# Kernel optimization log

Measured on AMD Instinct MI355X. Metric: run time of the kernel, lower is better.

Reference implementation:

```python
import jax, jax.numpy as jnp
import numpy as np

B, S, D, H = 64, 128, 1024, 512
N = 2 * S - 1          # total tree nodes (leaves + internal)
NSTEP = S - 1          # number of binary compositions
NW, NP = 511, 152      # word / phrase category counts


def _l2n(x):
    return x / jnp.clip(jnp.linalg.norm(x, axis=-1, keepdims=True), 1e-12)


def circular_correlation(a, b):
    a, b = _l2n(a), _l2n(b)
    c = jnp.fft.irfft(jnp.conj(jnp.fft.rfft(a)) * jnp.fft.rfft(b), n=H)
    return _l2n(c)


def _lstm_dir(x, w_ih, w_hh, b):
    # x: [B,S,D] -> hs: [B,S,H]; PyTorch gate order i,f,g,o
    xp = jnp.einsum('bsd,gd->bsg', x, w_ih) + b  # precompute input proj

    def step(carry, xt):
        h, c = carry
        g = xt + h @ w_hh.T
        i, f, gg, o = jnp.split(g, 4, axis=-1)
        c = jax.nn.sigmoid(f) * c + jax.nn.sigmoid(i) * jnp.tanh(gg)
        h = jax.nn.sigmoid(o) * jnp.tanh(c)
        return (h, c), h

    h0 = jnp.zeros((x.shape[0], H), x.dtype)
    _, hs = jax.lax.scan(step, (h0, h0), xp.transpose(1, 0, 2))
    return hs.transpose(1, 0, 2)


def setup_inputs():
    key = jax.random.key(0)
    ks = jax.random.split(key, 12)
    sc = 0.05
    elmo_rep = jax.random.normal(ks[0], (B, S, D), jnp.float32)
    w_ih_f = jax.random.normal(ks[1], (4 * H, D), jnp.float32) * sc
    w_hh_f = jax.random.normal(ks[2], (4 * H, H), jnp.float32) * sc
    b_f = jnp.zeros((4 * H,), jnp.float32)
    w_ih_b = jax.random.normal(ks[3], (4 * H, D), jnp.float32) * sc
    w_hh_b = jax.random.normal(ks[4], (4 * H, H), jnp.float32) * sc
    b_b = jnp.zeros((4 * H,), jnp.float32)
    W1 = jax.random.normal(ks[5], (H, H), jnp.float32) * sc
    W2 = jax.random.normal(ks[6], (H, H), jnp.float32) * sc
    word_W = jax.random.normal(ks[7], (NW, H), jnp.float32) * sc
    word_b = jnp.zeros((NW,), jnp.float32)
    phrase_W = jax.random.normal(ks[8], (NP, H), jnp.float32) * sc
    phrase_b = jnp.zeros((NP,), jnp.float32)
    # valid binary-tree composition schedule: parent S+i, children < S+i
    rng = np.random.default_rng(0)
    comp = np.zeros((B, NSTEP, 4), np.int32)
    comp[:, :, 0] = 2
    for i in range(NSTEP):
        comp[:, i, 1] = S + i
        comp[:, i, 2] = rng.integers(0, S + i, size=B)
        comp[:, i, 3] = rng.integers(0, S + i, size=B)
    composition_info = jnp.asarray(comp)
    pos = jnp.stack([jnp.arange(S), jnp.arange(S)], axis=1).astype(jnp.int32)
    original_pos = jnp.tile(pos[None], (B, 1, 1))
    batch_label = jax.random.randint(ks[9], (B, N), 0, NW, dtype=jnp.int64)
    return dict(elmo_rep=elmo_rep, w_ih_f=w_ih_f, w_hh_f=w_hh_f, b_f=b_f,
                w_ih_b=w_ih_b, w_hh_b=w_hh_b, b_b=b_b, W1=W1, W2=W2,
                word_W=word_W, word_b=word_b, phrase_W=phrase_W,
                phrase_b=phrase_b, composition_info=composition_info,
                original_pos=original_pos, batch_label=batch_label)


def reference(elmo_rep, w_ih_f, w_hh_f, b_f, w_ih_b, w_hh_b, b_b, W1, W2,
              word_W, word_b, phrase_W, phrase_b, composition_info,
              original_pos, batch_label):
    # BiLSTM over ELMo reps (all sequences full length S)
    fwd = _lstm_dir(elmo_rep, w_ih_f, w_hh_f, b_f)
    bwd = _lstm_dir(elmo_rep[:, ::-1], w_ih_b, w_hh_b, b_b)[:, ::-1]
    combined = jax.nn.leaky_relu(fwd @ W1.T + bwd @ W2.T, negative_slope=0.01)

    # scatter leaves into node buffer [B,N,H], then L2-normalize
    bidx = jnp.arange(B)[:, None]
    tgt = original_pos[:, :, 0]
    src = original_pos[:, :, 1]
    vector = jnp.zeros((B, N, H), combined.dtype)
    vector = vector.at[bidx, tgt].set(combined[bidx, src])
    vector = _l2n(vector)

    # sequential per-depth compose: gather children, circular-correlate, scatter parent
    b = jnp.arange(B)

    def step(vec, info):  # info: [B,4] = [type, parent, left, right]
        t, p, l, r = info[:, 0], info[:, 1], info[:, 2], info[:, 3]
        lv = vec[b, l]
        rv = vec[b, r]
        comp = circular_correlation(lv, rv)
        cur = vec[b, p]
        val = jnp.where((t == 1)[:, None], lv,
                        jnp.where((t == 2)[:, None], comp, cur))
        return vec.at[b, p].set(val), None

    vector, _ = jax.lax.scan(step, vector, composition_info.transpose(1, 0, 2))

    # words = leaf nodes (first S slots), phrases = internal nodes
    word_vector = vector[:, :S].reshape(-1, H)
    phrase_vector = vector[:, S:].reshape(-1, H)
    word_label = batch_label[:, :S].reshape(-1)
    phrase_label = batch_label[:, S:].reshape(-1)
    word_output = word_vector @ word_W.T + word_b
    phrase_output = phrase_vector @ phrase_W.T + phrase_b
    return word_output, phrase_output, word_label, phrase_label
```

## Files before the change

kernel.cpp:

```cpp
#include <hip/hip_runtime.h>
#include <math.h>

#define NB 64
#define NS 128
#define ND 1024
#define NH 512
#define NG 2048
#define NTOT 255
#define NSTEPS 127
#define NWV 511
#define NPV 152

static const size_t XPB_SZ = (size_t)2 * NS * NG * NB;
static const size_t H_SZ   = (size_t)2 * NS * NH * NB;
static const size_t VEC_SZ = (size_t)NB * NTOT * NH;
static const size_t HB_SZ  = (size_t)2 * NS * NH * NB;
static const size_t EB_SZ  = (size_t)NB * NS * ND;
static const size_t WB_SZ  = (size_t)4096 * ND;

typedef __attribute__((ext_vector_type(8))) short short8v;
typedef __attribute__((ext_vector_type(8))) unsigned short ushort8v;
typedef __attribute__((ext_vector_type(4))) float float4v;

__device__ __forceinline__ float sigm(float x) { return 1.f / (1.f + __expf(-x)); }
__device__ __forceinline__ float tanh_fast(float x) {
  const float e = __expf(2.f * x);
  return 1.f - 2.f / (e + 1.f);
}
__device__ __forceinline__ unsigned short f2bf(float x) {
  unsigned b = __float_as_uint(x);
  return (unsigned short)((b + 0x7FFFu + ((b >> 16) & 1u)) >> 16);
}
__device__ __forceinline__ float bf2f(unsigned short u) {
  return __uint_as_float(((unsigned)u) << 16);
}

#define FMA4x4(acc, av, bv)                                                    \
  acc[0][0] += av.x * bv.x; acc[0][1] += av.x * bv.y;                          \
  acc[0][2] += av.x * bv.z; acc[0][3] += av.x * bv.w;                          \
  acc[1][0] += av.y * bv.x; acc[1][1] += av.y * bv.y;                          \
  acc[1][2] += av.y * bv.z; acc[1][3] += av.y * bv.w;                          \
  acc[2][0] += av.z * bv.x; acc[2][1] += av.z * bv.y;                          \
  acc[2][2] += av.z * bv.z; acc[2][3] += av.z * bv.w;                          \
  acc[3][0] += av.w * bv.x; acc[3][1] += av.w * bv.y;                          \
  acc[3][2] += av.w * bv.z; acc[3][3] += av.w * bv.w;

__global__ __launch_bounds__(256) void k_cvt(
    const float* __restrict__ elmo, const float* __restrict__ wf,
    const float* __restrict__ wb, unsigned short* __restrict__ elmo_bf,
    unsigned short* __restrict__ W_bf, int* __restrict__ bar) {
  const int gid = blockIdx.x * 256 + threadIdx.x;
  if (gid < 8192) bar[gid] = 0;
  const int NE4 = (NB * NS * ND) / 4;
  const int NW4 = (4096 * ND) / 4;
  const int NW4h = NW4 / 2;
  for (int i = gid; i < NE4 + NW4; i += gridDim.x * 256) {
    float4 v;
    unsigned short* dst;
    if (i < NE4) {
      const int e0 = i << 2;
      const int b = e0 >> 17;
      const int t = (e0 >> 10) & 127;
      const int k = e0 & 1023;
      v = *(const float4*)(elmo + e0);
      dst = elmo_bf + ((size_t)((t << 6) + b) << 10) + k;
    } else {
      const int j = i - NE4;
      v = (j < NW4h) ? *(const float4*)(wf + ((size_t)j << 2))
                     : *(const float4*)(wb + ((size_t)(j - NW4h) << 2));
      dst = W_bf + ((size_t)j << 2);
    }
    uint2 u;
    u.x = (unsigned)f2bf(v.x) | ((unsigned)f2bf(v.y) << 16);
    u.y = (unsigned)f2bf(v.z) | ((unsigned)f2bf(v.w) << 16);
    *(uint2*)dst = u;
  }
}

__global__ __launch_bounds__(256) void k_xp(
    const unsigned short* __restrict__ elmo_bf,
    const unsigned short* __restrict__ W_bf,
    const float* __restrict__ biasf, const float* __restrict__ biasb,
    unsigned short* __restrict__ xpb) {
  __shared__ unsigned short As[128 * 64];
  __shared__ unsigned short Bs[128 * 64];
  const int tid = threadIdx.x;
  const int n0 = blockIdx.x * 128;
  const int m0 = blockIdx.y * 128;
  const int wv = tid >> 6, lane = tid & 63;
  const int cl = lane & 15, bq = lane >> 4;
  const int wm = (wv >> 1) << 6;
  const int wn = (wv & 1) << 6;
  const int sr = tid >> 1, skc = (tid & 1) << 5;
  const unsigned short* asrc = elmo_bf + (size_t)(m0 + sr) * ND + skc;
  const unsigned short* bsrc = W_bf + (size_t)(n0 + sr) * ND + skc;
  const int sswz = (sr & 15) << 3;
  float4v acc[4][4];
#pragma unroll
  for (int nt = 0; nt < 4; ++nt) {
    const int n = n0 + wn + nt * 16 + cl;
    const float bv = (n < 2048) ? biasf[n] : biasb[n - 2048];
#pragma unroll
    for (int mt = 0; mt < 4; ++mt) acc[mt][nt] = (float4v){bv, bv, bv, bv};
  }
  for (int k0 = 0; k0 < ND; k0 += 64) {
    ushort8v av4[4], bv4[4];
#pragma unroll
    for (int i = 0; i < 4; ++i) av4[i] = *(const ushort8v*)(asrc + k0 + 8 * i);
#pragma unroll
    for (int i = 0; i < 4; ++i) bv4[i] = *(const ushort8v*)(bsrc + k0 + 8 * i);
    __syncthreads();
#pragma unroll
    for (int i = 0; i < 4; ++i) {
      *(ushort8v*)&As[((sr << 6) + skc + 8 * i) ^ sswz] = av4[i];
      *(ushort8v*)&Bs[((sr << 6) + skc + 8 * i) ^ sswz] = bv4[i];
    }
    __syncthreads();
#pragma unroll
    for (int ks = 0; ks < 2; ++ks) {
      const int koff = (ks << 5) + (bq << 3);
      short8v af[4], bf_[4];
#pragma unroll
      for (int mt = 0; mt < 4; ++mt) {
        const int ar = wm + mt * 16 + cl;
        af[mt] = *(const short8v*)&As[((ar << 6) + koff) ^ ((ar & 15) << 3)];
      }
#pragma unroll
      for (int nt = 0; nt < 4; ++nt) {
        const int br = wn + nt * 16 + cl;
        bf_[nt] = *(const short8v*)&Bs[((br << 6) + koff) ^ ((br & 15) << 3)];
      }
#pragma unroll
      for (int mt = 0; mt < 4; ++mt)
#pragma unroll
        for (int nt = 0; nt < 4; ++nt)
          acc[mt][nt] =
              __builtin_amdgcn_mfma_f32_16x16x32_bf16(af[mt], bf_[nt], acc[mt][nt], 0, 0, 0);
    }
  }
#pragma unroll
  for (int mt = 0; mt < 4; ++mt) {
    const int mbase = m0 + wm + mt * 16 + (bq << 2);
    const int t = mbase >> 6, b4 = mbase & 63;
#pragma unroll
    for (int nt = 0; nt < 4; ++nt) {
      const int n = n0 + wn + nt * 16 + cl;
      const int dir = n >> 11, grow = n & 2047;
      const int g = grow >> 9, cb = (grow & 511) >> 4;
      const float4v a = acc[mt][nt];
      uint2 u;
      u.x = (unsigned)f2bf(a[0]) | ((unsigned)f2bf(a[1]) << 16);
      u.y = (unsigned)f2bf(a[2]) | ((unsigned)f2bf(a[3]) << 16);
      const size_t idx =
          ((((size_t)(dir * NS + t) * 32 + cb) * 4 + g) << 10) + (cl << 6) + b4;
      *(uint2*)&xpb[idx] = u;
    }
  }
}

__global__ __launch_bounds__(256) void k_lstm(
    const float* __restrict__ whh_f, const float* __restrict__ whh_b,
    const unsigned short* __restrict__ xpb, float* __restrict__ h_all,
    unsigned short* __restrict__ h_bf, int* __restrict__ bar) {
  __shared__ unsigned short WS[64 * 512];
  __shared__ unsigned short hOut[64 * 16];
  const int bid = blockIdx.x;
  const int dir = bid >> 5;
  const int cb = bid & 31;
  const int col0 = cb << 4;
  const int tid = threadIdx.x;
  const int lane = tid & 63;
  const int w = tid >> 6;
  const int cl = lane & 15, bq = lane >> 4;
  const int b4 = (w << 4) + (bq << 2);
  const int arow = (w << 4) + cl;
  const float* whh = dir ? whh_b : whh_f;

  {
    const int gr = tid >> 2;
    const int kc = (tid & 3) << 7;
    const int gg = gr >> 4, cc = gr & 15;
    const float* src = whh + (size_t)(gg * NH + col0 + cc) * NH + kc;
    const int swz = (gr & 15) << 3;
#pragma unroll
    for (int i = 0; i < 16; ++i) {
      const float4 f0 = *(const float4*)(src + 8 * i);
      const float4 f1 = *(const float4*)(src + 8 * i + 4);
      ushort8v u;
      u[0] = f2bf(f0.x); u[1] = f2bf(f0.y); u[2] = f2bf(f0.z); u[3] = f2bf(f0.w);
      u[4] = f2bf(f1.x); u[5] = f2bf(f1.y); u[6] = f2bf(f1.z); u[7] = f2bf(f1.w);
      *(ushort8v*)&WS[((gr << 9) + kc + 8 * i) ^ swz] = u;
    }
  }
  __syncthreads();

  float* hd = h_all + (size_t)dir * NS * NH * NB;
  unsigned short* hb_us = h_bf + ((size_t)dir * NS << 15);
  unsigned long long* hb_ull = (unsigned long long*)h_bf + ((size_t)dir * NS << 12);

  float4v c4 = {0.f, 0.f, 0.f, 0.f};

  uint2 xg0, xg1, xg2, xg3;
  {
    const int pos0 = dir ? (NS - 1) : 0;
    const unsigned short* xc = xpb + (((size_t)(dir * NS + pos0) * 32 + cb) << 12);
    xg0 = *(const uint2*)&xc[(0 << 10) + (cl << 6) + b4];
    xg1 = *(const uint2*)&xc[(1 << 10) + (cl << 6) + b4];
    xg2 = *(const uint2*)&xc[(2 << 10) + (cl << 6) + b4];
    xg3 = *(const uint2*)&xc[(3 << 10) + (cl << 6) + b4];
  }

  for (int t = 0; t < NS; ++t) {
    const int pos = dir ? (NS - 1 - t) : t;
    float4v acc[4] = {{0.f, 0.f, 0.f, 0.f}, {0.f, 0.f, 0.f, 0.f},
                      {0.f, 0.f, 0.f, 0.f}, {0.f, 0.f, 0.f, 0.f}};
    if (t > 0) {
      const int prevpos = dir ? (pos + 1) : (pos - 1);
      const unsigned long long* hsrc = hb_ull + ((size_t)prevpos << 13);
      unsigned long long ha0[16], ha1[16];
#pragma unroll
      for (int ks = 0; ks < 16; ++ks) {
        const int uidx = (arow << 7) + (ks << 3) + (bq << 1);
        ha0[ks] = __hip_atomic_load(&hsrc[uidx], __ATOMIC_RELAXED,
                                    __HIP_MEMORY_SCOPE_AGENT);
        ha1[ks] = __hip_atomic_load(&hsrc[uidx + 1], __ATOMIC_RELAXED,
                                    __HIP_MEMORY_SCOPE_AGENT);
      }
#pragma unroll
      for (int ks = 0; ks < 16; ++ks) {
        union { unsigned long long u[2]; short8v v; } au;
        au.u[0] = ha0[ks]; au.u[1] = ha1[ks];
        const short8v a = au.v;
        const int koff = (ks << 5) + (bq << 3);
#pragma unroll
        for (int g = 0; g < 4; ++g) {
          const short8v bb =
              *(const short8v*)&WS[((((g << 4) + cl) << 9) + koff) ^ (cl << 3)];
          acc[g] = __builtin_amdgcn_mfma_f32_16x16x32_bf16(a, bb, acc[g], 0, 0, 0);
        }
      }
    }
    float hv[4];
#pragma unroll
    for (int i = 0; i < 4; ++i) {
      const unsigned xw0 = (i < 2) ? xg0.x : xg0.y;
      const unsigned xw1 = (i < 2) ? xg1.x : xg1.y;
      const unsigned xw2 = (i < 2) ? xg2.x : xg2.y;
      const unsigned xw3 = (i < 2) ? xg3.x : xg3.y;
      const int sh = (i & 1) << 4;
      const float gi = sigm(acc[0][i] + bf2f((unsigned short)(xw0 >> sh)));
      const float gf = sigm(acc[1][i] + bf2f((unsigned short)(xw1 >> sh)));
      const float gc = tanh_fast(acc[2][i] + bf2f((unsigned short)(xw2 >> sh)));
      const float go = sigm(acc[3][i] + bf2f((unsigned short)(xw3 >> sh)));
      c4[i] = gf * c4[i] + gi * gc;
      hv[i] = go * tanh_fast(c4[i]);
    }
    *(float4*)(hd + ((size_t)pos * NH + col0 + cl) * NB + b4) =
        make_float4(hv[0], hv[1], hv[2], hv[3]);
    if (t < NS - 1) {
#pragma unroll
      for (int i = 0; i < 4; ++i) hOut[((b4 + i) << 4) + cl] = f2bf(hv[i]);
      const int npos = dir ? (pos - 1) : (pos + 1);
      const unsigned short* xc =
          xpb + (((size_t)(dir * NS + npos) * 32 + cb) << 12);
      const uint2 nx0 = *(const uint2*)&xc[(0 << 10) + (cl << 6) + b4];
      const uint2 nx1 = *(const uint2*)&xc[(1 << 10) + (cl << 6) + b4];
      const uint2 nx2 = *(const uint2*)&xc[(2 << 10) + (cl << 6) + b4];
      const uint2 nx3 = *(const uint2*)&xc[(3 << 10) + (cl << 6) + b4];
      __syncthreads();
      if (tid < 128) {
        const int bb = tid >> 1, half = tid & 1;
        const unsigned long long v =
            *(const unsigned long long*)&hOut[(bb << 4) + (half << 3)];
        __hip_atomic_store(
            (unsigned long long*)&hb_us[((size_t)pos << 15) + (bb << 9) + col0 +
                                        (half << 3)],
            v, __ATOMIC_RELAXED, __HIP_MEMORY_SCOPE_AGENT);
      }
      __syncthreads();
      if (tid == 0) {
        int* ctr = &bar[(((t << 1) + dir) << 5)];
        __hip_atomic_fetch_add(ctr, 1, __ATOMIC_RELAXED, __HIP_MEMORY_SCOPE_AGENT);
        while (__hip_atomic_load(ctr, __ATOMIC_RELAXED, __HIP_MEMORY_SCOPE_AGENT) < 32) {
        }
      }
      __syncthreads();
      xg0 = nx0; xg1 = nx1; xg2 = nx2; xg3 = nx3;
    }
  }
}

__global__ __launch_bounds__(256) void k_comb(
    const float* __restrict__ h_all, const float* __restrict__ W1,
    const float* __restrict__ W2, float* __restrict__ vec) {
  __shared__ float A1[16][68], A2[16][68], B1[16][68], B2[16][68];
  const int tid = threadIdx.x;
  const int n0 = blockIdx.x * 64;
  const int s = blockIdx.y;
  const float* h0 = h_all + (size_t)s * NH * NB;
  const float* h1 = h_all + ((size_t)NS + s) * NH * NB;
  const int aj = tid >> 4, ai4 = (tid & 15) << 2;
  const int lr = tid >> 2, lc4 = (tid & 3) << 2;
  const int tx = tid & 15, ty = tid >> 4;
  const float* b1row = W1 + (size_t)(n0 + lr) * NH;
  const float* b2row = W2 + (size_t)(n0 + lr) * NH;
  float acc[4][4] = {};
  for (int k0 = 0; k0 < NH; k0 += 16) {
    *(float4*)&A1[aj][ai4] = *(const float4*)(h0 + (size_t)(k0 + aj) * NB + ai4);
    *(float4*)&A2[aj][ai4] = *(const float4*)(h1 + (size_t)(k0 + aj) * NB + ai4);
    const float4 w1 = *(const float4*)(b1row + k0 + lc4);
    B1[lc4 + 0][lr] = w1.x; B1[lc4 + 1][lr] = w1.y;
    B1[lc4 + 2][lr] = w1.z; B1[lc4 + 3][lr] = w1.w;
    const float4 w2 = *(const float4*)(b2row + k0 + lc4);
    B2[lc4 + 0][lr] = w2.x; B2[lc4 + 1][lr] = w2.y;
    B2[lc4 + 2][lr] = w2.z; B2[lc4 + 3][lr] = w2.w;
    __syncthreads();
#pragma unroll
    for (int kk = 0; kk < 16; ++kk) {
      const float4 a1 = *(const float4*)&A1[kk][ty << 2];
      const float4 b1 = *(const float4*)&B1[kk][tx << 2];
      FMA4x4(acc, a1, b1)
      const float4 a2 = *(const float4*)&A2[kk][ty << 2];
      const float4 b2 = *(const float4*)&B2[kk][tx << 2];
      FMA4x4(acc, a2, b2)
    }
    __syncthreads();
  }
#pragma unroll
  for (int i = 0; i < 4; ++i) {
    const int b = (ty << 2) + i;
#pragma unroll
    for (int j = 0; j < 4; ++j) {
      const int nn = n0 + (tx << 2) + j;
      float v = acc[i][j];
      v = v > 0.f ? v : 0.01f * v;
      vec[((size_t)b * NTOT + s) * NH + nn] = v;
    }
  }
}

__global__ __launch_bounds__(256) void k_norm(float* __restrict__ vec) {
  const int row = (blockIdx.x << 2) + (threadIdx.x >> 6);
  const int lane = threadIdx.x & 63;
  const int b = row >> 7, s = row & 127;
  float* p = vec + ((size_t)b * NTOT + s) * NH;
  float4 v0 = *(float4*)(p + (lane << 3));
  float4 v1 = *(float4*)(p + (lane << 3) + 4);
  float ss = v0.x * v0.x + v0.y * v0.y + v0.z * v0.z + v0.w * v0.w +
             v1.x * v1.x + v1.y * v1.y + v1.z * v1.z + v1.w * v1.w;
#pragma unroll
  for (int off = 32; off; off >>= 1) ss += __shfl_down(ss, off);
  ss = __shfl(ss, 0);
  const float sc = 1.f / fmaxf(sqrtf(ss), 1e-12f);
  v0.x *= sc; v0.y *= sc; v0.z *= sc; v0.w *= sc;
  v1.x *= sc; v1.y *= sc; v1.z *= sc; v1.w *= sc;
  *(float4*)(p + (lane << 3)) = v0;
  *(float4*)(p + (lane << 3) + 4) = v1;
}

#define SKW(f) ((f) + (((f) >> 5) << 2))
__global__ __launch_bounds__(512) void k_compose(
    float* __restrict__ vec, const int* __restrict__ cinfo) {
  __shared__ float lv[512];
  __shared__ float rvd[1152];
  __shared__ float cpart[8 * 576];
  __shared__ float red[8];
  const int b = blockIdx.x;
  const int tid = threadIdx.x;
  float* vb = vec + (size_t)b * NTOT * NH;
  const int* ib = cinfo + b * NSTEPS * 4;
  const int jq = tid >> 6;
  const int jb = jq << 6;
  const int k8 = (tid & 63) << 3;
  const int wid = tid >> 6, lane = tid & 63;
  for (int i = 0; i < NSTEPS; ++i) {
    const int tt = ib[i * 4 + 0], p = ib[i * 4 + 1];
    const int l = ib[i * 4 + 2], r = ib[i * 4 + 3];
    const float lvv = vb[(size_t)l * NH + tid];
    const float rvv = vb[(size_t)r * NH + tid];
    lv[tid] = lvv;
    rvd[SKW(tid)] = rvv;
    rvd[SKW(512 + tid)] = rvv;
    __syncthreads();
    if (tt == 2) {
      float acc[8] = {};
#pragma unroll 4
      for (int jj = 0; jj < 64; jj += 4) {
        const int j = jb + jj;
        const float4 l4 = *(const float4*)&lv[j];
        const int f0 = j + k8;
        const float4 r0 = *(const float4*)&rvd[SKW(f0)];
        const float4 r1 = *(const float4*)&rvd[SKW(f0 + 4)];
        const float4 r2 = *(const float4*)&rvd[SKW(f0 + 8)];
        const float rw[12] = {r0.x, r0.y, r0.z, r0.w, r1.x, r1.y,
                              r1.z, r1.w, r2.x, r2.y, r2.z, r2.w};
#pragma unroll
        for (int kk = 0; kk < 8; ++kk)
          acc[kk] += l4.x * rw[kk] + l4.y * rw[kk + 1] + l4.z * rw[kk + 2] +
                     l4.w * rw[kk + 3];
      }
      const int ca = jq * 576 + SKW(k8);
      *(float4*)&cpart[ca] = make_float4(acc[0], acc[1], acc[2], acc[3]);
      *(float4*)&cpart[ca + 4] = make_float4(acc[4], acc[5], acc[6], acc[7]);
    }
    __syncthreads();
    float ck = 0.f;
    if (tt == 2) {
      const int ra = SKW(tid);
#pragma unroll
      for (int q = 0; q < 8; ++q) ck += cpart[q * 576 + ra];
    }
    float ss = ck * ck;
#pragma unroll
    for (int off = 32; off; off >>= 1) ss += __shfl_xor(ss, off);
    if (lane == 0) red[wid] = ss;
    __syncthreads();
    if (tt == 2) {
      const float tot = red[0] + red[1] + red[2] + red[3] +
                        red[4] + red[5] + red[6] + red[7];
      const float inv = 1.f / fmaxf(sqrtf(tot), 1e-12f);
      vb[(size_t)p * NH + tid] = ck * inv;
    } else if (tt == 1) {
      vb[(size_t)p * NH + tid] = lvv;
    }
    __syncthreads();
  }
}

template <int MODE>
__global__ __launch_bounds__(256) void k_out(
    const float* __restrict__ vec, const float* __restrict__ W,
    const float* __restrict__ bias, float* __restrict__ out) {
  constexpr int NOUT = MODE ? NPV : NWV;
  __shared__ float As[16][68], Bs[16][68];
  const int tid = threadIdx.x;
  const int n0 = blockIdx.x * 64, m0 = blockIdx.y * 64;
  const int lr = tid >> 2, lc4 = (tid & 3) << 2;
  const int tx = tid & 15, ty = tid >> 4;
  const int m = m0 + lr;
  int vr;
  if (MODE == 0) {
    vr = (m >> 7) * NTOT + (m & 127);
  } else {
    const int bb = m / 127;
    vr = bb * NTOT + NS + (m - bb * 127);
  }
  const float* arow = vec + (size_t)vr * NH;
  const int n = n0 + lr;
  const float* brow = W + (size_t)n * NH;
  const bool bok = (n < NOUT);
  float acc[4][4] = {};
  for (int k0 = 0; k0 < NH; k0 += 16) {
    const float4 a4 = *(const float4*)(arow + k0 + lc4);
    As[lc4 + 0][lr] = a4.x; As[lc4 + 1][lr] = a4.y;
    As[lc4 + 2][lr] = a4.z; As[lc4 + 3][lr] = a4.w;
    float4 b4 = make_float4(0.f, 0.f, 0.f, 0.f);
    if (bok) b4 = *(const float4*)(brow + k0 + lc4);
    Bs[lc4 + 0][lr] = b4.x; Bs[lc4 + 1][lr] = b4.y;
    Bs[lc4 + 2][lr] = b4.z; Bs[lc4 + 3][lr] = b4.w;
    __syncthreads();
#pragma unroll
    for (int kk = 0; kk < 16; ++kk) {
      const float4 av = *(const float4*)&As[kk][ty << 2];
      const float4 bv = *(const float4*)&Bs[kk][tx << 2];
      FMA4x4(acc, av, bv)
    }
    __syncthreads();
  }
#pragma unroll
  for (int i = 0; i < 4; ++i)
#pragma unroll
    for (int j = 0; j < 4; ++j) {
      const int nn = n0 + (tx << 2) + j;
      if (nn < NOUT)
        out[(size_t)(m0 + (ty << 2) + i) * NOUT + nn] = acc[i][j] + bias[nn];
    }
}

__global__ __launch_bounds__(256) void k_labels(
    const int* __restrict__ lab, float* __restrict__ outw,
    float* __restrict__ outp) {
  const int i = blockIdx.x * 256 + threadIdx.x;
  if (i < NB * NS) {
    const int b = i >> 7, s = i & 127;
    outw[i] = (float)lab[b * NTOT + s];
  }
  if (i < NB * NSTEPS) {
    const int b = i / 127;
    outp[i] = (float)lab[b * NTOT + NS + (i - b * 127)];
  }
}

extern "C" void kernel_launch(void* const* d_in, const int* in_sizes, int n_in,
                              void* d_out, int out_size, void* d_ws, size_t ws_size,
                              hipStream_t stream) {
  (void)in_sizes; (void)n_in; (void)out_size; (void)ws_size;
  const float* elmo     = (const float*)d_in[0];
  const float* w_ih_f   = (const float*)d_in[1];
  const float* w_hh_f   = (const float*)d_in[2];
  const float* b_f      = (const float*)d_in[3];
  const float* w_ih_b   = (const float*)d_in[4];
  const float* w_hh_b   = (const float*)d_in[5];
  const float* b_b      = (const float*)d_in[6];
  const float* W1       = (const float*)d_in[7];
  const float* W2       = (const float*)d_in[8];
  const float* word_W   = (const float*)d_in[9];
  const float* word_b   = (const float*)d_in[10];
  const float* phrase_W = (const float*)d_in[11];
  const float* phrase_b = (const float*)d_in[12];
  const int* cinfo      = (const int*)d_in[13];
  const int* lab        = (const int*)d_in[15];

  unsigned short* xpb  = (unsigned short*)d_ws;
  float* h_all         = (float*)(xpb + XPB_SZ);
  float* vec           = h_all + H_SZ;
  unsigned short* h_bf = (unsigned short*)(vec + VEC_SZ);
  unsigned short* e_bf = h_bf + HB_SZ;
  unsigned short* W_bf = e_bf + EB_SZ;
  int* bar             = (int*)(W_bf + WB_SZ);

  float* out_word = (float*)d_out;
  float* out_phr  = out_word + (size_t)8192 * NWV;
  float* out_lw   = out_phr + (size_t)8128 * NPV;
  float* out_lp   = out_lw + 8192;

  k_cvt<<<dim3(2048), 256, 0, stream>>>(elmo, w_ih_f, w_ih_b, e_bf, W_bf, bar);
  k_xp<<<dim3(32, 64), 256, 0, stream>>>(e_bf, W_bf, b_f, b_b, xpb);
  k_lstm<<<dim3(64), 256, 0, stream>>>(w_hh_f, w_hh_b, xpb, h_all, h_bf, bar);
  k_comb<<<dim3(8, 128), 256, 0, stream>>>(h_all, W1, W2, vec);
  k_norm<<<dim3(2048), 256, 0, stream>>>(vec);
  k_compose<<<dim3(64), 512, 0, stream>>>(vec, cinfo);
  k_out<0><<<dim3(8, 128), 256, 0, stream>>>(vec, word_W, word_b, out_word);
  k_out<1><<<dim3(3, 127), 256, 0, stream>>>(vec, phrase_W, phrase_b, out_phr);
  k_labels<<<dim3(32), 256, 0, stream>>>(lab, out_lw, out_lp);
}
```

Baseline: 1.691 ms.

## Use bf16 MFMA for combine and word-output GEMMs, drop fp32 LSTM output

The combine GEMM (h·W1 + h·W2) and the word-output GEMM move from fp32 scalar FMA tiles to bf16 MFMA tiles with swizzled shared memory. The LSTM no longer writes fp32 hidden states. It keeps only the bf16 copy and adds a final-step store so every position is present for the combine kernel. W1/W2 and word_W are converted to bf16 in the existing conversion kernel, and the norm kernel also emits a bf16 copy of leaf vectors. This trades fp32 precision for bf16 in these GEMMs and cuts memory traffic.

```diff
diff --git a/kernel.cpp b/kernel.cpp
--- a/kernel.cpp
+++ b/kernel.cpp
@@ -17,6 +17,9 @@
 static const size_t HB_SZ  = (size_t)2 * NS * NH * NB;
 static const size_t EB_SZ  = (size_t)NB * NS * ND;
 static const size_t WB_SZ  = (size_t)4096 * ND;
+static const size_t W12_SZ = (size_t)2 * NH * NH;
+static const size_t WO_SZ  = (size_t)512 * NH;
+static const size_t VB_SZ  = (size_t)NB * NS * NH;
 
 typedef __attribute__((ext_vector_type(8))) short short8v;
 typedef __attribute__((ext_vector_type(8))) unsigned short ushort8v;
@@ -47,15 +50,22 @@
 
 __global__ __launch_bounds__(256) void k_cvt(
     const float* __restrict__ elmo, const float* __restrict__ wf,
-    const float* __restrict__ wb, unsigned short* __restrict__ elmo_bf,
-    unsigned short* __restrict__ W_bf, int* __restrict__ bar) {
+    const float* __restrict__ wb, const float* __restrict__ W1,
+    const float* __restrict__ W2, const float* __restrict__ wordW,
+    unsigned short* __restrict__ elmo_bf, unsigned short* __restrict__ W_bf,
+    unsigned short* __restrict__ W12_bf, unsigned short* __restrict__ wout_bf,
+    int* __restrict__ bar) {
   const int gid = blockIdx.x * 256 + threadIdx.x;
   if (gid < 8192) bar[gid] = 0;
   const int NE4 = (NB * NS * ND) / 4;
   const int NW4 = (4096 * ND) / 4;
   const int NW4h = NW4 / 2;
-  for (int i = gid; i < NE4 + NW4; i += gridDim.x * 256) {
-    float4 v;
+  const int N12 = (int)(W12_SZ / 4);
+  const int NWO = (int)(WO_SZ / 4);
+  const int NWO_real = (NWV * NH) / 4;
+  const int TOT = NE4 + NW4 + N12 + NWO;
+  for (int i = gid; i < TOT; i += gridDim.x * 256) {
+    float4 v = make_float4(0.f, 0.f, 0.f, 0.f);
     unsigned short* dst;
     if (i < NE4) {
       const int e0 = i << 2;
@@ -64,11 +74,21 @@
       const int k = e0 & 1023;
       v = *(const float4*)(elmo + e0);
       dst = elmo_bf + ((size_t)((t << 6) + b) << 10) + k;
-    } else {
+    } else if (i < NE4 + NW4) {
       const int j = i - NE4;
       v = (j < NW4h) ? *(const float4*)(wf + ((size_t)j << 2))
                      : *(const float4*)(wb + ((size_t)(j - NW4h) << 2));
       dst = W_bf + ((size_t)j << 2);
+    } else if (i < NE4 + NW4 + N12) {
+      const int j = i - NE4 - NW4;
+      const int half = N12 / 2;
+      v = (j < half) ? *(const float4*)(W1 + ((size_t)j << 2))
+                     : *(const float4*)(W2 + ((size_t)(j - half) << 2));
+      dst = W12_bf + ((size_t)j << 2);
+    } else {
+      const int j = i - NE4 - NW4 - N12;
+      if (j < NWO_real) v = *(const float4*)(wordW + ((size_t)j << 2));
+      dst = wout_bf + ((size_t)j << 2);
     }
     uint2 u;
     u.x = (unsigned)f2bf(v.x) | ((unsigned)f2bf(v.y) << 16);
@@ -160,7 +180,7 @@
 
 __global__ __launch_bounds__(256) void k_lstm(
     const float* __restrict__ whh_f, const float* __restrict__ whh_b,
-    const unsigned short* __restrict__ xpb, float* __restrict__ h_all,
+    const unsigned short* __restrict__ xpb,
     unsigned short* __restrict__ h_bf, int* __restrict__ bar) {
   __shared__ unsigned short WS[64 * 512];
   __shared__ unsigned short hOut[64 * 16];
@@ -194,7 +214,6 @@
   }
   __syncthreads();
 
-  float* hd = h_all + (size_t)dir * NS * NH * NB;
   unsigned short* hb_us = h_bf + ((size_t)dir * NS << 15);
   unsigned long long* hb_ull = (unsigned long long*)h_bf + ((size_t)dir * NS << 12);
 
@@ -255,11 +274,9 @@
       c4[i] = gf * c4[i] + gi * gc;
       hv[i] = go * tanh_fast(c4[i]);
     }
-    *(float4*)(hd + ((size_t)pos * NH + col0 + cl) * NB + b4) =
-        make_float4(hv[0], hv[1], hv[2], hv[3]);
+#pragma unroll
+    for (int i = 0; i < 4; ++i) hOut[((b4 + i) << 4) + cl] = f2bf(hv[i]);
     if (t < NS - 1) {
-#pragma unroll
-      for (int i = 0; i < 4; ++i) hOut[((b4 + i) << 4) + cl] = f2bf(hv[i]);
       const int npos = dir ? (pos - 1) : (pos + 1);
       const unsigned short* xc =
           xpb + (((size_t)(dir * NS + npos) * 32 + cb) << 12);
@@ -286,60 +303,92 @@
       }
       __syncthreads();
       xg0 = nx0; xg1 = nx1; xg2 = nx2; xg3 = nx3;
+    } else {
+      __syncthreads();
+      if (tid < 128) {
+        const int bb = tid >> 1, half = tid & 1;
+        const unsigned long long v =
+            *(const unsigned long long*)&hOut[(bb << 4) + (half << 3)];
+        __hip_atomic_store(
+            (unsigned long long*)&hb_us[((size_t)pos << 15) + (bb << 9) + col0 +
+                                        (half << 3)],
+            v, __ATOMIC_RELAXED, __HIP_MEMORY_SCOPE_AGENT);
+      }
     }
   }
 }
 
 __global__ __launch_bounds__(256) void k_comb(
-    const float* __restrict__ h_all, const float* __restrict__ W1,
-    const float* __restrict__ W2, float* __restrict__ vec) {
-  __shared__ float A1[16][68], A2[16][68], B1[16][68], B2[16][68];
+    const unsigned short* __restrict__ h_bf,
+    const unsigned short* __restrict__ W12_bf, float* __restrict__ vec) {
+  __shared__ unsigned short A1s[64 * 128], A2s[64 * 128];
+  __shared__ unsigned short B1s[64 * 128], B2s[64 * 128];
   const int tid = threadIdx.x;
   const int n0 = blockIdx.x * 64;
   const int s = blockIdx.y;
-  const float* h0 = h_all + (size_t)s * NH * NB;
-  const float* h1 = h_all + ((size_t)NS + s) * NH * NB;
-  const int aj = tid >> 4, ai4 = (tid & 15) << 2;
-  const int lr = tid >> 2, lc4 = (tid & 3) << 2;
-  const int tx = tid & 15, ty = tid >> 4;
-  const float* b1row = W1 + (size_t)(n0 + lr) * NH;
-  const float* b2row = W2 + (size_t)(n0 + lr) * NH;
-  float acc[4][4] = {};
-  for (int k0 = 0; k0 < NH; k0 += 16) {
-    *(float4*)&A1[aj][ai4] = *(const float4*)(h0 + (size_t)(k0 + aj) * NB + ai4);
-    *(float4*)&A2[aj][ai4] = *(const float4*)(h1 + (size_t)(k0 + aj) * NB + ai4);
-    const float4 w1 = *(const float4*)(b1row + k0 + lc4);
-    B1[lc4 + 0][lr] = w1.x; B1[lc4 + 1][lr] = w1.y;
-    B1[lc4 + 2][lr] = w1.z; B1[lc4 + 3][lr] = w1.w;
-    const float4 w2 = *(const float4*)(b2row + k0 + lc4);
-    B2[lc4 + 0][lr] = w2.x; B2[lc4 + 1][lr] = w2.y;
-    B2[lc4 + 2][lr] = w2.z; B2[lc4 + 3][lr] = w2.w;
-    __syncthreads();
-#pragma unroll
-    for (int kk = 0; kk < 16; ++kk) {
-      const float4 a1 = *(const float4*)&A1[kk][ty << 2];
-      const float4 b1 = *(const float4*)&B1[kk][tx << 2];
-      FMA4x4(acc, a1, b1)
-      const float4 a2 = *(const float4*)&A2[kk][ty << 2];
-      const float4 b2 = *(const float4*)&B2[kk][tx << 2];
-      FMA4x4(acc, a2, b2)
-    }
-    __syncthreads();
-  }
-#pragma unroll
-  for (int i = 0; i < 4; ++i) {
-    const int b = (ty << 2) + i;
-#pragma unroll
-    for (int j = 0; j < 4; ++j) {
-      const int nn = n0 + (tx << 2) + j;
-      float v = acc[i][j];
+  const int w = tid >> 6, lane = tid & 63;
+  const int cl = lane & 15, bq = lane >> 4;
+  const int wn = w << 4;
+  const unsigned short* a1src = h_bf + ((size_t)s << 15);
+  const unsigned short* a2src = h_bf + ((size_t)(NS + s) << 15);
+  const unsigned short* b1src = W12_bf + (size_t)n0 * NH;
+  const unsigned short* b2src = W12_bf + (size_t)(NH + n0) * NH;
+  const int srow = tid >> 2, skq = (tid & 3) << 5;
+  const int sswz = (srow & 15) << 3;
+  float4v acc[4] = {{0.f, 0.f, 0.f, 0.f}, {0.f, 0.f, 0.f, 0.f},
+                    {0.f, 0.f, 0.f, 0.f}, {0.f, 0.f, 0.f, 0.f}};
+  for (int k0 = 0; k0 < NH; k0 += 128) {
+    ushort8v a1[4], a2[4], b1[4], b2[4];
+#pragma unroll
+    for (int i = 0; i < 4; ++i) {
+      const size_t off = (size_t)srow * NH + k0 + skq + 8 * i;
+      a1[i] = *(const ushort8v*)(a1src + off);
+      a2[i] = *(const ushort8v*)(a2src + off);
+      b1[i] = *(const ushort8v*)(b1src + off);
+      b2[i] = *(const ushort8v*)(b2src + off);
+    }
+    __syncthreads();
+#pragma unroll
+    for (int i = 0; i < 4; ++i) {
+      const int idx = ((srow << 7) + skq + 8 * i) ^ sswz;
+      *(ushort8v*)&A1s[idx] = a1[i];
+      *(ushort8v*)&A2s[idx] = a2[i];
+      *(ushort8v*)&B1s[idx] = b1[i];
+      *(ushort8v*)&B2s[idx] = b2[i];
+    }
+    __syncthreads();
+#pragma unroll
+    for (int ks = 0; ks < 4; ++ks) {
+      const int koff = (ks << 5) + (bq << 3);
+      const short8v bf1 =
+          *(const short8v*)&B1s[(((wn + cl) << 7) + koff) ^ (cl << 3)];
+      const short8v bf2 =
+          *(const short8v*)&B2s[(((wn + cl) << 7) + koff) ^ (cl << 3)];
+#pragma unroll
+      for (int mt = 0; mt < 4; ++mt) {
+        const int ar = mt * 16 + cl;
+        const short8v af1 = *(const short8v*)&A1s[((ar << 7) + koff) ^ (cl << 3)];
+        const short8v af2 = *(const short8v*)&A2s[((ar << 7) + koff) ^ (cl << 3)];
+        acc[mt] = __builtin_amdgcn_mfma_f32_16x16x32_bf16(af1, bf1, acc[mt], 0, 0, 0);
+        acc[mt] = __builtin_amdgcn_mfma_f32_16x16x32_bf16(af2, bf2, acc[mt], 0, 0, 0);
+      }
+    }
+  }
+  const int n = n0 + wn + cl;
+#pragma unroll
+  for (int mt = 0; mt < 4; ++mt) {
+    const int b0 = mt * 16 + (bq << 2);
+#pragma unroll
+    for (int i = 0; i < 4; ++i) {
+      float v = acc[mt][i];
       v = v > 0.f ? v : 0.01f * v;
-      vec[((size_t)b * NTOT + s) * NH + nn] = v;
-    }
-  }
-}
-
-__global__ __launch_bounds__(256) void k_norm(float* __restrict__ vec) {
+      vec[((size_t)(b0 + i) * NTOT + s) * NH + n] = v;
+    }
+  }
+}
+
+__global__ __launch_bounds__(256) void k_norm(float* __restrict__ vec,
+                                              unsigned short* __restrict__ vec_bf) {
   const int row = (blockIdx.x << 2) + (threadIdx.x >> 6);
   const int lane = threadIdx.x & 63;
   const int b = row >> 7, s = row & 127;
@@ -356,6 +405,10 @@
   v1.x *= sc; v1.y *= sc; v1.z *= sc; v1.w *= sc;
   *(float4*)(p + (lane << 3)) = v0;
   *(float4*)(p + (lane << 3) + 4) = v1;
+  ushort8v u;
+  u[0] = f2bf(v0.x); u[1] = f2bf(v0.y); u[2] = f2bf(v0.z); u[3] = f2bf(v0.w);
+  u[4] = f2bf(v1.x); u[5] = f2bf(v1.y); u[6] = f2bf(v1.z); u[7] = f2bf(v1.w);
+  *(ushort8v*)&vec_bf[((size_t)row << 9) + (lane << 3)] = u;
 }
 
 #define SKW(f) ((f) + (((f) >> 5) << 2))
@@ -427,24 +480,87 @@
   }
 }
 
-template <int MODE>
-__global__ __launch_bounds__(256) void k_out(
+__global__ __launch_bounds__(256) void k_outw(
+    const unsigned short* __restrict__ vec_bf,
+    const unsigned short* __restrict__ wout_bf,
+    const float* __restrict__ bias, float* __restrict__ out) {
+  __shared__ unsigned short As[128 * 64];
+  __shared__ unsigned short Bs[128 * 64];
+  const int tid = threadIdx.x;
+  const int n0 = blockIdx.x * 128;
+  const int m0 = blockIdx.y * 128;
+  const int wv = tid >> 6, lane = tid & 63;
+  const int cl = lane & 15, bq = lane >> 4;
+  const int wm = (wv >> 1) << 6;
+  const int wn = (wv & 1) << 6;
+  const int sr = tid >> 1, skc = (tid & 1) << 5;
+  const unsigned short* asrc = vec_bf + (size_t)(m0 + sr) * NH + skc;
+  const unsigned short* bsrc = wout_bf + (size_t)(n0 + sr) * NH + skc;
+  const int sswz = (sr & 15) << 3;
+  float4v acc[4][4] = {};
+  for (int k0 = 0; k0 < NH; k0 += 64) {
+    ushort8v av4[4], bv4[4];
+#pragma unroll
+    for (int i = 0; i < 4; ++i) av4[i] = *(const ushort8v*)(asrc + k0 + 8 * i);
+#pragma unroll
+    for (int i = 0; i < 4; ++i) bv4[i] = *(const ushort8v*)(bsrc + k0 + 8 * i);
+    __syncthreads();
+#pragma unroll
+    for (int i = 0; i < 4; ++i) {
+      *(ushort8v*)&As[((sr << 6) + skc + 8 * i) ^ sswz] = av4[i];
+      *(ushort8v*)&Bs[((sr << 6) + skc + 8 * i) ^ sswz] = bv4[i];
+    }
+    __syncthreads();
+#pragma unroll
+    for (int ks = 0; ks < 2; ++ks) {
+      const int koff = (ks << 5) + (bq << 3);
+      short8v af[4], bf_[4];
+#pragma unroll
+      for (int mt = 0; mt < 4; ++mt) {
+        const int ar = wm + mt * 16 + cl;
+        af[mt] = *(const short8v*)&As[((ar << 6) + koff) ^ ((ar & 15) << 3)];
+      }
+#pragma unroll
+      for (int nt = 0; nt < 4; ++nt) {
+        const int br = wn + nt * 16 + cl;
+        bf_[nt] = *(const short8v*)&Bs[((br << 6) + koff) ^ ((br & 15) << 3)];
+      }
+#pragma unroll
+      for (int mt = 0; mt < 4; ++mt)
+#pragma unroll
+        for (int nt = 0; nt < 4; ++nt)
+          acc[mt][nt] =
+              __builtin_amdgcn_mfma_f32_16x16x32_bf16(af[mt], bf_[nt], acc[mt][nt], 0, 0, 0);
+    }
+  }
+#pragma unroll
+  for (int mt = 0; mt < 4; ++mt) {
+    const int mb = m0 + wm + mt * 16 + (bq << 2);
+#pragma unroll
+    for (int nt = 0; nt < 4; ++nt) {
+      const int n = n0 + wn + nt * 16 + cl;
+      if (n < NWV) {
+        const float bn = bias[n];
+#pragma unroll
+        for (int i = 0; i < 4; ++i)
+          out[(size_t)(mb + i) * NWV + n] = acc[mt][nt][i] + bn;
+      }
+    }
+  }
+}
+
+__global__ __launch_bounds__(256) void k_outp(
     const float* __restrict__ vec, const float* __restrict__ W,
     const float* __restrict__ bias, float* __restrict__ out) {
-  constexpr int NOUT = MODE ? NPV : NWV;
+  constexpr int NOUT = NPV;
   __shared__ float As[16][68], Bs[16][68];
   const int tid = threadIdx.x;
   const int n0 = blockIdx.x * 64, m0 = blockIdx.y * 64;
   const int lr = tid >> 2, lc4 = (tid & 3) << 2;
   const int tx = tid & 15, ty = tid >> 4;
   const int m = m0 + lr;
-  int vr;
-  if (MODE == 0) {
-    vr = (m >> 7) * NTOT + (m & 127);
-  } else {
-    const int bb = m / 127;
-    vr = bb * NTOT + NS + (m - bb * 127);
-  }
+  const int bb = m / 127;
+  const int vr = bb * NTOT + NS + (m - bb * 127);
   const float* arow = vec + (size_t)vr * NH;
   const int n = n0 + lr;
   const float* brow = W + (size_t)n * NH;
@@ -511,26 +627,30 @@
   const int* cinfo      = (const int*)d_in[13];
   const int* lab        = (const int*)d_in[15];
 
-  unsigned short* xpb  = (unsigned short*)d_ws;
-  float* h_all         = (float*)(xpb + XPB_SZ);
-  float* vec           = h_all + H_SZ;
-  unsigned short* h_bf = (unsigned short*)(vec + VEC_SZ);
-  unsigned short* e_bf = h_bf + HB_SZ;
-  unsigned short* W_bf = e_bf + EB_SZ;
-  int* bar             = (int*)(W_bf + WB_SZ);
+  unsigned short* xpb   = (unsigned short*)d_ws;
+  float* h_all          = (float*)(xpb + XPB_SZ);
+  float* vec            = h_all + H_SZ;
+  unsigned short* h_bf  = (unsigned short*)(vec + VEC_SZ);
+  unsigned short* e_bf  = h_bf + HB_SZ;
+  unsigned short* W_bf  = e_bf + EB_SZ;
+  unsigned short* W12_bf  = W_bf + WB_SZ;
+  unsigned short* wout_bf = W12_bf + W12_SZ;
+  unsigned short* vec_bf  = wout_bf + WO_SZ;
+  int* bar              = (int*)(vec_bf + VB_SZ);
 
   float* out_word = (float*)d_out;
   float* out_phr  = out_word + (size_t)8192 * NWV;
   float* out_lw   = out_phr + (size_t)8128 * NPV;
   float* out_lp   = out_lw + 8192;
 
-  k_cvt<<<dim3(2048), 256, 0, stream>>>(elmo, w_ih_f, w_ih_b, e_bf, W_bf, bar);
+  k_cvt<<<dim3(2048), 256, 0, stream>>>(elmo, w_ih_f, w_ih_b, W1, W2, word_W,
+                                        e_bf, W_bf, W12_bf, wout_bf, bar);
   k_xp<<<dim3(32, 64), 256, 0, stream>>>(e_bf, W_bf, b_f, b_b, xpb);
-  k_lstm<<<dim3(64), 256, 0, stream>>>(w_hh_f, w_hh_b, xpb, h_all, h_bf, bar);
-  k_comb<<<dim3(8, 128), 256, 0, stream>>>(h_all, W1, W2, vec);
-  k_norm<<<dim3(2048), 256, 0, stream>>>(vec);
+  k_lstm<<<dim3(64), 256, 0, stream>>>(w_hh_f, w_hh_b, xpb, h_bf, bar);
+  k_comb<<<dim3(8, 128), 256, 0, stream>>>(h_bf, W12_bf, vec);
+  k_norm<<<dim3(2048), 256, 0, stream>>>(vec, vec_bf);
   k_compose<<<dim3(64), 512, 0, stream>>>(vec, cinfo);
-  k_out<0><<<dim3(8, 128), 256, 0, stream>>>(vec, word_W, word_b, out_word);
-  k_out<1><<<dim3(3, 127), 256, 0, stream>>>(vec, phrase_W, phrase_b, out_phr);
+  k_outw<<<dim3(4, 64), 256, 0, stream>>>(vec_bf, wout_bf, word_b, out_word);
+  k_outp<<<dim3(3, 127), 256, 0, stream>>>(vec, phrase_W, phrase_b, out_phr);
   k_labels<<<dim3(32), 256, 0, stream>>>(lab, out_lw, out_lp);
 }
```

Result: faster. 1.556 ms (-7.9%).
